# Optimization experiments

Measured on AMD Instinct MI355X. Metric: run time of the kernel, lower is better.

## Reference

```python
import jax, jax.numpy as jnp
import numpy as np

NUM_BINS = 16

def _compute_histogram(colors, num_bins=NUM_BINS):
    # colors: (N, 3) in [0, 1]
    quantized = (colors * (num_bins - 1)).astype(jnp.int32)
    quantized = jnp.clip(quantized, 0, num_bins - 1)
    # flatten 3D bin index: r*B^2 + g*B + b
    flat_idx = (quantized[:, 0] * num_bins + quantized[:, 1]) * num_bins + quantized[:, 2]
    hist = jax.ops.segment_sum(
        jnp.ones(colors.shape[0], dtype=colors.dtype),
        flat_idx,
        num_segments=num_bins ** 3,
    )
    hist = hist / (hist.sum() + 1e-8)
    return hist  # (num_bins^3,)

def setup_inputs() -> dict:
    key = jax.random.key(0)
    k1, k2 = jax.random.split(key)
    source_colors = jax.random.uniform(k1, (8388608, 3), dtype=jnp.float32)
    target_palette = jax.random.uniform(k2, (4096, 3), dtype=jnp.float32)
    return {"source_colors": source_colors, "target_palette": target_palette}

def reference(source_colors, target_palette):
    source_hist = _compute_histogram(source_colors)
    target_hist = _compute_histogram(target_palette)
    loss = jnp.abs(source_hist - target_hist).mean()
    return loss
```

## Files before the change

### kernel.cpp

```cpp
#include <hip/hip_runtime.h>

#define BINS 4096
#define WORDS 2048
#define H_GRID 1024
#define H_BLOCK 256
#define CHUNKS 8

__device__ __forceinline__ int qz(float c) {
    int q = (int)(c * 15.0f);
    q = q < 0 ? 0 : q;
    q = q > 15 ? 15 : q;
    return q;
}

__device__ __forceinline__ int bin3(float r, float g, float b) {
    return (qz(r) << 8) | (qz(g) << 4) | qz(b);
}

__global__ __launch_bounds__(H_BLOCK) void hist_partial_kernel(
        const float* __restrict__ src, unsigned int* __restrict__ partials,
        int n_pts) {
    __shared__ unsigned int lh[WORDS];
    for (int i = threadIdx.x; i < WORDS; i += H_BLOCK) lh[i] = 0;
    __syncthreads();

    const float4* __restrict__ src4 = (const float4*)src;
    const int n_quads = n_pts >> 2;
    const int tid = blockIdx.x * H_BLOCK + threadIdx.x;
    const int stride = gridDim.x * H_BLOCK;
    for (int q = tid; q < n_quads; q += stride) {
        float4 a = src4[3 * q + 0];
        float4 b = src4[3 * q + 1];
        float4 c = src4[3 * q + 2];
        int b0 = bin3(a.x, a.y, a.z);
        int b1 = bin3(a.w, b.x, b.y);
        int b2 = bin3(b.z, b.w, c.x);
        int b3 = bin3(c.y, c.z, c.w);
        atomicAdd(&lh[b0 >> 1], 1u << ((b0 & 1) << 4));
        atomicAdd(&lh[b1 >> 1], 1u << ((b1 & 1) << 4));
        atomicAdd(&lh[b2 >> 1], 1u << ((b2 & 1) << 4));
        atomicAdd(&lh[b3 >> 1], 1u << ((b3 & 1) << 4));
    }
    if (blockIdx.x == 0) {
        int tail = n_pts & 3;
        if ((int)threadIdx.x < tail) {
            int p = (n_quads << 2) + threadIdx.x;
            int bb = bin3(src[3 * p], src[3 * p + 1], src[3 * p + 2]);
            atomicAdd(&lh[bb >> 1], 1u << ((bb & 1) << 4));
        }
    }
    __syncthreads();

    uint4* dst = (uint4*)(partials + (size_t)blockIdx.x * WORDS);
    const uint4* lh4 = (const uint4*)lh;
#pragma unroll
    for (int p = 0; p < WORDS / (H_BLOCK * 4); ++p)
        dst[threadIdx.x + p * H_BLOCK] = lh4[threadIdx.x + p * H_BLOCK];
}

__global__ __launch_bounds__(256) void reduce_kernel(
        const unsigned int* __restrict__ partials,
        unsigned int* __restrict__ g_part) {
    const int bin   = (blockIdx.x & 15) * 256 + threadIdx.x;
    const int chunk = blockIdx.x >> 4;
    const int r0    = chunk * (H_GRID / CHUNKS);
    const unsigned short* __restrict__ p16 = (const unsigned short*)partials;
    unsigned int s = 0;
#pragma unroll 8
    for (int r = 0; r < H_GRID / CHUNKS; ++r)
        s += (unsigned int)p16[(size_t)(r0 + r) * BINS + bin];
    g_part[chunk * BINS + bin] = s;
}

__global__ __launch_bounds__(1024) void loss_kernel(
        const float* __restrict__ tgt, const unsigned int* __restrict__ g_part,
        float* __restrict__ out, int n_src, int n_tgt) {
    __shared__ unsigned int th[BINS];
    for (int i = threadIdx.x; i < BINS; i += 1024) th[i] = 0;
    __syncthreads();

    const float4* __restrict__ t4 = (const float4*)tgt;
    const int tq = n_tgt >> 2;
    for (int q = threadIdx.x; q < tq; q += 1024) {
        float4 a = t4[3 * q + 0];
        float4 b = t4[3 * q + 1];
        float4 c = t4[3 * q + 2];
        atomicAdd(&th[bin3(a.x, a.y, a.z)], 1u);
        atomicAdd(&th[bin3(a.w, b.x, b.y)], 1u);
        atomicAdd(&th[bin3(b.z, b.w, c.x)], 1u);
        atomicAdd(&th[bin3(c.y, c.z, c.w)], 1u);
    }
    {
        int tail = n_tgt & 3;
        if ((int)threadIdx.x < tail) {
            int p = (tq << 2) + threadIdx.x;
            atomicAdd(&th[bin3(tgt[3 * p], tgt[3 * p + 1], tgt[3 * p + 2])], 1u);
        }
    }
    __syncthreads();

    const double ns = (double)n_src + 1e-8;
    const double nt = (double)n_tgt + 1e-8;
    double acc = 0.0;
    for (int i = threadIdx.x; i < BINS; i += 1024) {
        unsigned int sv = 0;
#pragma unroll
        for (int c = 0; c < CHUNKS; ++c) sv += g_part[c * BINS + i];
        acc += fabs((double)sv / ns - (double)th[i] / nt);
    }

    for (int off = 32; off > 0; off >>= 1) acc += __shfl_down(acc, off);
    __shared__ double red[16];
    if ((threadIdx.x & 63) == 0) red[threadIdx.x >> 6] = acc;
    __syncthreads();
    if (threadIdx.x == 0) {
        double s = 0.0;
        for (int w = 0; w < 16; ++w) s += red[w];
        out[0] = (float)(s / (double)BINS);
    }
}

extern "C" void kernel_launch(void* const* d_in, const int* in_sizes, int n_in,
                              void* d_out, int out_size, void* d_ws, size_t ws_size,
                              hipStream_t stream) {
    const float* src = (const float*)d_in[0];
    const float* tgt = (const float*)d_in[1];
    const int n_src = in_sizes[0] / 3;
    const int n_tgt = in_sizes[1] / 3;

    unsigned int* partials = (unsigned int*)d_ws;
    unsigned int* g_part   = partials + (size_t)H_GRID * WORDS;

    hist_partial_kernel<<<H_GRID, H_BLOCK, 0, stream>>>(src, partials, n_src);
    reduce_kernel<<<16 * CHUNKS, 256, 0, stream>>>(partials, g_part);
    loss_kernel<<<1, 1024, 0, stream>>>(tgt, g_part, (float*)d_out, n_src, n_tgt);
}
```

Measured before the change: 153.5 us.

## Fuse reduce and loss kernels via last-block counter; unroll histogram loop by two

Merges the partial-histogram reduction and the loss computation into one kernel. A global atomic counter picks the last finishing block, which then builds the target histogram and computes the loss, so one kernel launch goes away. The histogram loop now processes two strided quads per iteration to issue more loads before the LDS atomics. The trade-off is that the final stage runs on a 256-thread block instead of 1024 threads, and it adds fences plus an atomic.

```diff
diff --git a/kernel.cpp b/kernel.cpp
--- a/kernel.cpp
+++ b/kernel.cpp
@@ -5,6 +5,8 @@
 #define H_GRID 1024
 #define H_BLOCK 256
 #define CHUNKS 8
+#define R_GRID (16 * CHUNKS)
+#define R_BLOCK 256
 
 __device__ __forceinline__ int qz(float c) {
     int q = (int)(c * 15.0f);
@@ -17,9 +19,14 @@
     return (qz(r) << 8) | (qz(g) << 4) | qz(b);
 }
 
+__device__ __forceinline__ void lds_count(unsigned int* lh, int b) {
+    atomicAdd(&lh[b >> 1], 1u << ((b & 1) << 4));
+}
+
 __global__ __launch_bounds__(H_BLOCK) void hist_partial_kernel(
         const float* __restrict__ src, unsigned int* __restrict__ partials,
-        int n_pts) {
+        unsigned int* __restrict__ counter, int n_pts) {
+    if (blockIdx.x == 0 && threadIdx.x == 0) *counter = 0;
     __shared__ unsigned int lh[WORDS];
     for (int i = threadIdx.x; i < WORDS; i += H_BLOCK) lh[i] = 0;
     __syncthreads();
@@ -28,25 +35,39 @@
     const int n_quads = n_pts >> 2;
     const int tid = blockIdx.x * H_BLOCK + threadIdx.x;
     const int stride = gridDim.x * H_BLOCK;
-    for (int q = tid; q < n_quads; q += stride) {
+
+    int q = tid;
+    for (; q + stride < n_quads; q += 2 * stride) {
+        float4 a0 = src4[3 * q + 0];
+        float4 b0 = src4[3 * q + 1];
+        float4 c0 = src4[3 * q + 2];
+        int q1 = q + stride;
+        float4 a1 = src4[3 * q1 + 0];
+        float4 b1 = src4[3 * q1 + 1];
+        float4 c1 = src4[3 * q1 + 2];
+        lds_count(lh, bin3(a0.x, a0.y, a0.z));
+        lds_count(lh, bin3(a0.w, b0.x, b0.y));
+        lds_count(lh, bin3(b0.z, b0.w, c0.x));
+        lds_count(lh, bin3(c0.y, c0.z, c0.w));
+        lds_count(lh, bin3(a1.x, a1.y, a1.z));
+        lds_count(lh, bin3(a1.w, b1.x, b1.y));
+        lds_count(lh, bin3(b1.z, b1.w, c1.x));
+        lds_count(lh, bin3(c1.y, c1.z, c1.w));
+    }
+    for (; q < n_quads; q += stride) {
         float4 a = src4[3 * q + 0];
         float4 b = src4[3 * q + 1];
         float4 c = src4[3 * q + 2];
-        int b0 = bin3(a.x, a.y, a.z);
-        int b1 = bin3(a.w, b.x, b.y);
-        int b2 = bin3(b.z, b.w, c.x);
-        int b3 = bin3(c.y, c.z, c.w);
-        atomicAdd(&lh[b0 >> 1], 1u << ((b0 & 1) << 4));
-        atomicAdd(&lh[b1 >> 1], 1u << ((b1 & 1) << 4));
-        atomicAdd(&lh[b2 >> 1], 1u << ((b2 & 1) << 4));
-        atomicAdd(&lh[b3 >> 1], 1u << ((b3 & 1) << 4));
+        lds_count(lh, bin3(a.x, a.y, a.z));
+        lds_count(lh, bin3(a.w, b.x, b.y));
+        lds_count(lh, bin3(b.z, b.w, c.x));
+        lds_count(lh, bin3(c.y, c.z, c.w));
     }
     if (blockIdx.x == 0) {
         int tail = n_pts & 3;
         if ((int)threadIdx.x < tail) {
             int p = (n_quads << 2) + threadIdx.x;
-            int bb = bin3(src[3 * p], src[3 * p + 1], src[3 * p + 2]);
-            atomicAdd(&lh[bb >> 1], 1u << ((bb & 1) << 4));
+            lds_count(lh, bin3(src[3 * p], src[3 * p + 1], src[3 * p + 2]));
         }
     }
     __syncthreads();
@@ -58,10 +79,12 @@
         dst[threadIdx.x + p * H_BLOCK] = lh4[threadIdx.x + p * H_BLOCK];
 }
 
-__global__ __launch_bounds__(256) void reduce_kernel(
+__global__ __launch_bounds__(R_BLOCK) void reduce_loss_kernel(
         const unsigned int* __restrict__ partials,
-        unsigned int* __restrict__ g_part) {
-    const int bin   = (blockIdx.x & 15) * 256 + threadIdx.x;
+        unsigned int* __restrict__ g_part, unsigned int* __restrict__ counter,
+        const float* __restrict__ tgt, float* __restrict__ out,
+        int n_src, int n_tgt) {
+    const int bin   = (blockIdx.x & 15) * R_BLOCK + threadIdx.x;
     const int chunk = blockIdx.x >> 4;
     const int r0    = chunk * (H_GRID / CHUNKS);
     const unsigned short* __restrict__ p16 = (const unsigned short*)partials;
@@ -70,18 +93,24 @@
     for (int r = 0; r < H_GRID / CHUNKS; ++r)
         s += (unsigned int)p16[(size_t)(r0 + r) * BINS + bin];
     g_part[chunk * BINS + bin] = s;
-}
 
-__global__ __launch_bounds__(1024) void loss_kernel(
-        const float* __restrict__ tgt, const unsigned int* __restrict__ g_part,
-        float* __restrict__ out, int n_src, int n_tgt) {
+    __threadfence();
+    __syncthreads();
+    __shared__ int is_last;
+    if (threadIdx.x == 0) {
+        unsigned int prev = atomicAdd(counter, 1u);
+        is_last = (prev == (unsigned int)(R_GRID - 1)) ? 1 : 0;
+    }
+    __syncthreads();
+    if (!is_last) return;
+    __threadfence();
+
     __shared__ unsigned int th[BINS];
-    for (int i = threadIdx.x; i < BINS; i += 1024) th[i] = 0;
+    for (int i = threadIdx.x; i < BINS; i += R_BLOCK) th[i] = 0;
     __syncthreads();
-
     const float4* __restrict__ t4 = (const float4*)tgt;
     const int tq = n_tgt >> 2;
-    for (int q = threadIdx.x; q < tq; q += 1024) {
+    for (int q = threadIdx.x; q < tq; q += R_BLOCK) {
         float4 a = t4[3 * q + 0];
         float4 b = t4[3 * q + 1];
         float4 c = t4[3 * q + 2];
@@ -102,21 +131,20 @@
     const double ns = (double)n_src + 1e-8;
     const double nt = (double)n_tgt + 1e-8;
     double acc = 0.0;
-    for (int i = threadIdx.x; i < BINS; i += 1024) {
+    for (int i = threadIdx.x; i < BINS; i += R_BLOCK) {
         unsigned int sv = 0;
 #pragma unroll
         for (int c = 0; c < CHUNKS; ++c) sv += g_part[c * BINS + i];
         acc += fabs((double)sv / ns - (double)th[i] / nt);
     }
-
     for (int off = 32; off > 0; off >>= 1) acc += __shfl_down(acc, off);
-    __shared__ double red[16];
+    __shared__ double red[R_BLOCK / 64];
     if ((threadIdx.x & 63) == 0) red[threadIdx.x >> 6] = acc;
     __syncthreads();
     if (threadIdx.x == 0) {
-        double s = 0.0;
-        for (int w = 0; w < 16; ++w) s += red[w];
-        out[0] = (float)(s / (double)BINS);
+        double t = 0.0;
+        for (int w = 0; w < R_BLOCK / 64; ++w) t += red[w];
+        out[0] = (float)(t / (double)BINS);
     }
 }
 
@@ -130,8 +158,9 @@
 
     unsigned int* partials = (unsigned int*)d_ws;
     unsigned int* g_part   = partials + (size_t)H_GRID * WORDS;
+    unsigned int* counter  = g_part + CHUNKS * BINS;
 
-    hist_partial_kernel<<<H_GRID, H_BLOCK, 0, stream>>>(src, partials, n_src);
-    reduce_kernel<<<16 * CHUNKS, 256, 0, stream>>>(partials, g_part);
-    loss_kernel<<<1, 1024, 0, stream>>>(tgt, g_part, (float*)d_out, n_src, n_tgt);
+    hist_partial_kernel<<<H_GRID, H_BLOCK, 0, stream>>>(src, partials, counter, n_src);
+    reduce_loss_kernel<<<R_GRID, R_BLOCK, 0, stream>>>(
+        partials, g_part, counter, tgt, (float*)d_out, n_src, n_tgt);
 }
```

Result: slower. 167.7 us (+9.3%).
